# Kernel optimization log

Measured on AMD Instinct MI355X. Metric: run time of the kernel, lower is better.

Reference implementation:

```python
import jax, jax.numpy as jnp
import numpy as np

WIN = 8          # current_window
PRETRAIN = 8     # pretrain_window
HEADS = 8
SHIFT = WIN // 2 # shift_size, shift_dir = [1, 1] (shift_mode=1)
L = WIN * WIN
LOG100 = float(np.log(100.0))


def _shift_mask(H, W):
    # bands (shift_dir=[1,1], no padding). Pairs from different regions get -100.
    hr = np.repeat(np.arange(3), [H - WIN, WIN - SHIFT, SHIFT])
    wr = np.repeat(np.arange(3), [W - WIN, WIN - SHIFT, SHIFT])
    region = hr[:, None] * 3 + wr[None, :]                      # [H, W]
    reg = region.reshape(H // WIN, WIN, W // WIN, WIN)
    reg = reg.transpose(0, 2, 1, 3).reshape(-1, L)              # [nw, L]
    m = np.where(reg[:, :, None] != reg[:, None, :], -100.0, 0.0)
    return jnp.asarray(m, dtype=jnp.float32)[None, :, None]     # [1, nw, 1, L, L]


def _rel_bias(cpb_w1, cpb_b1, cpb_w2):
    # Swin-v2 continuous relative position bias (log-spaced coords + MLP).
    pos = np.stack(np.meshgrid(np.arange(WIN), np.arange(WIN), indexing='ij'), -1).reshape(L, 2)
    rc = (pos[:, None, :] - pos[None, :, :]).astype(np.float32)  # [L, L, 2]
    rc = rc / (PRETRAIN - 1) * 8.0
    rc = np.sign(rc) * np.log2(np.abs(rc) + 1.0) / np.log2(8.0)
    rc = jnp.asarray(rc)
    bias = jax.nn.relu(rc @ cpb_w1 + cpb_b1) @ cpb_w2            # [L, L, heads]
    bias = 16.0 * jax.nn.sigmoid(bias)
    return bias.transpose(2, 0, 1)                               # [heads, L, L]


def _l2n(a):
    # tf.math.l2_normalize with epsilon=1.55e-5
    return a * jax.lax.rsqrt(jnp.maximum(jnp.sum(a * a, -1, keepdims=True), 1.55e-5))


def setup_inputs() -> dict:
    key = jax.random.key(0)
    ks = jax.random.split(key, 6)
    B, H, W, C = 16, 128, 128, 256
    cpb = 512
    return {
        'x': jax.random.normal(ks[0], (B, H, W, C), jnp.float32),
        'qkv_w': jax.random.normal(ks[1], (C, 3 * C), jnp.float32) * 0.02,
        'q_bias': jnp.zeros((C,), jnp.float32),
        'v_bias': jnp.zeros((C,), jnp.float32),
        'scale': jnp.full((HEADS, 1, 1), np.log(10.0), jnp.float32),
        'cpb_w1': jax.random.normal(ks[2], (2, cpb), jnp.float32) * 0.02,
        'cpb_b1': jnp.zeros((cpb,), jnp.float32),
        'cpb_w2': jax.random.normal(ks[3], (cpb, HEADS), jnp.float32) * 0.02,
        'proj_w': jax.random.normal(ks[4], (C, C), jnp.float32) * 0.02,
        'proj_b': jnp.zeros((C,), jnp.float32),
    }


def reference(x, qkv_w, q_bias, v_bias, scale, cpb_w1, cpb_b1, cpb_w2, proj_w, proj_b):
    B, H, W, C = x.shape
    units = C // HEADS
    # qkv 1x1 conv + (q, 0, v) bias
    bias = jnp.concatenate([q_bias, jnp.zeros_like(q_bias), v_bias])
    qkv = jnp.einsum('bhwc,cd->bhwd', x, qkv_w) + bias
    # cyclic shift (H, W > window so shift is applied; no padding needed)
    qkv = jnp.roll(qkv, (-SHIFT, -SHIFT), axis=(1, 2))
    # fused window partition -> [B, nw, heads, L, 3*units]
    nh, nw = H // WIN, W // WIN
    t = qkv.reshape(B, nh, WIN, nw, WIN, HEADS, 3 * units)
    t = t.transpose(0, 1, 3, 5, 2, 4, 6).reshape(B, nh * nw, HEADS, L, 3 * units)
    q, k, v = jnp.split(t, 3, axis=-1)
    # cosine attention with clamped learned logit scale
    logit_scale = jnp.exp(jnp.minimum(scale, LOG100))            # [heads, 1, 1]
    attn = jnp.einsum('bnhld,bnhmd->bnhlm', _l2n(q) * logit_scale, _l2n(k))
    attn = attn + _rel_bias(cpb_w1, cpb_b1, cpb_w2)[None, None] + _shift_mask(H, W)
    attn = jax.nn.softmax(attn, axis=-1)
    out = jnp.einsum('bnhlm,bnhmd->bnhld', attn, v)
    # reverse partition, reverse shift, output projection
    out = out.reshape(B, nh, nw, HEADS, WIN, WIN, units)
    out = out.transpose(0, 1, 4, 2, 5, 3, 6).reshape(B, H, W, C)
    out = jnp.roll(out, (SHIFT, SHIFT), axis=(1, 2))
    return jnp.einsum('bhwc,cd->bhwd', out, proj_w) + proj_b
```

## Files before the change

### kernel.cpp

```cpp
#include <hip/hip_runtime.h>

typedef __attribute__((ext_vector_type(4))) float  f32x4;
typedef __attribute__((ext_vector_type(8))) __bf16 bf16x8;
typedef __attribute__((ext_vector_type(4))) __bf16 bf16x4;

__global__ __launch_bounds__(256) void prep_kernel(
    const float* __restrict__ qw, const float* __restrict__ pw,
    const float* __restrict__ qb, const float* __restrict__ vb,
    const float* __restrict__ w1, const float* __restrict__ b1,
    const float* __restrict__ w2,
    __bf16* __restrict__ W2, __bf16* __restrict__ Wp,
    float* __restrict__ bcat, float* __restrict__ cpbias)
{
  if (blockIdx.x < 131) {
    int i = blockIdx.x * 256 + threadIdx.x;
    if (i < 24576) {
      int h = i / 3072, rem = i - h * 3072;
      int ft = rem >> 9, rem2 = rem & 511;
      int ks = rem2 >> 6, l = rem2 & 63;
      int g = l >> 4, c = l & 15;
      int col = h * 96 + ft * 16 + c;
      bf16x8 v;
      #pragma unroll
      for (int j = 0; j < 8; ++j)
        v[j] = (__bf16)qw[(ks * 32 + g * 8 + j) * 768 + col];
      *(bf16x8*)(W2 + (size_t)i * 8) = v;
    } else if (i < 24576 + 8192) {
      int j = i - 24576;
      int wv = j >> 10, rem = j & 1023;
      int ft = rem >> 9, rem2 = rem & 511;
      int ks = rem2 >> 6, l = rem2 & 63;
      int g = l >> 4, c = l & 15;
      int col = wv * 32 + ft * 16 + c;
      bf16x8 v;
      #pragma unroll
      for (int j8 = 0; j8 < 8; ++j8)
        v[j8] = (__bf16)pw[(ks * 32 + g * 8 + j8) * 256 + col];
      *(bf16x8*)(Wp + (size_t)j * 8) = v;
    } else if (i < 24576 + 8192 + 768) {
      int cdx = i - 24576 - 8192;
      bcat[cdx] = (cdx < 256) ? qb[cdx] : ((cdx < 512) ? 0.0f : vb[cdx - 512]);
    }
  } else {
    int pair = (blockIdx.x - 131) * 256 + threadIdx.x;
    int lq = pair >> 6, mk = pair & 63;
    float d0 = (float)((lq >> 3) - (mk >> 3));
    float d1 = (float)((lq & 7) - (mk & 7));
    float v0 = d0 * (8.0f / 7.0f);
    float v1 = d1 * (8.0f / 7.0f);
    float s0 = (v0 > 0.f) ? 1.f : ((v0 < 0.f) ? -1.f : 0.f);
    float s1 = (v1 > 0.f) ? 1.f : ((v1 < 0.f) ? -1.f : 0.f);
    float r0 = s0 * log2f(fabsf(v0) + 1.0f) * (1.0f / 3.0f);
    float r1 = s1 * log2f(fabsf(v1) + 1.0f) * (1.0f / 3.0f);
    float acc[8] = {0.f, 0.f, 0.f, 0.f, 0.f, 0.f, 0.f, 0.f};
    #pragma unroll 4
    for (int j = 0; j < 512; ++j) {
      float h = fmaxf(r0 * w1[j] + r1 * w1[512 + j] + b1[j], 0.0f);
      #pragma unroll
      for (int q = 0; q < 8; ++q) acc[q] += h * w2[j * 8 + q];
    }
    #pragma unroll
    for (int q = 0; q < 8; ++q) {
      float s = 16.0f / (1.0f + __expf(-acc[q]));
      cpbias[(q * 64 + lq) * 64 + mk] = s;
    }
  }
}

__device__ __forceinline__ int win_region(int tok, int wi, int wj) {
  int r = tok >> 3, cc = tok & 7;
  int rh = (wi == 15) ? ((r < 4) ? 1 : 2) : 0;
  int rw = (wj == 15) ? ((cc < 4) ? 1 : 2) : 0;
  return rh * 3 + rw;
}

template <int FT>
__device__ __forceinline__ void qkv2(const __bf16* __restrict__ Wh,
                                     const __bf16* xs, int l, int g, int c,
                                     f32x4 (&a)[2][4])
{
  const f32x4 zz = {0.f, 0.f, 0.f, 0.f};
  #pragma unroll
  for (int ft = 0; ft < 2; ++ft)
    #pragma unroll
    for (int tt = 0; tt < 4; ++tt) a[ft][tt] = zz;
  #pragma unroll
  for (int ks = 0; ks < 8; ++ks) {
    bf16x8 w0 = *(const bf16x8*)(Wh + (size_t)(((FT + 0) * 8 + ks) * 64 + l) * 8);
    bf16x8 w1 = *(const bf16x8*)(Wh + (size_t)(((FT + 1) * 8 + ks) * 64 + l) * 8);
    #pragma unroll
    for (int tt = 0; tt < 4; ++tt) {
      int phys = (ks * 4 + g) ^ (c & 7);
      bf16x8 xf = *(const bf16x8*)&xs[(tt * 16 + c) * 256 + phys * 8];
      a[0][tt] = __builtin_amdgcn_mfma_f32_16x16x32_bf16(w0, xf, a[0][tt], 0, 0, 0);
      a[1][tt] = __builtin_amdgcn_mfma_f32_16x16x32_bf16(w1, xf, a[1][tt], 0, 0, 0);
    }
  }
}

__global__ __launch_bounds__(512, 2) void fused_kernel(
    const float* __restrict__ x, const __bf16* __restrict__ W2,
    const __bf16* __restrict__ Wp, const float* __restrict__ bcat,
    const float* __restrict__ scale, const float* __restrict__ cpb,
    const float* __restrict__ pb, float* __restrict__ outf)
{
  __shared__ __align__(16) __bf16 xs[64 * 256];
  __shared__ __align__(16) __bf16 vst[8][64 * 36];
  const f32x4 zz = {0.f, 0.f, 0.f, 0.f};

  int t = threadIdx.x;
  int h = t >> 6, l = t & 63, g = l >> 4, c = l & 15;
  int win = blockIdx.x, b = blockIdx.y;
  int wi = win >> 4, wj = win & 15;
  bool edge = (wi == 15) || (wj == 15);

  {
    int r = t >> 3;
    int q8 = t & 7;
    int ht = (wi * 8 + (r >> 3) + 4) & 127;
    int wt = (wj * 8 + (r & 7) + 4) & 127;
    const float* src = x + (size_t)((b * 128 + ht) * 128 + wt) * 256 + q8 * 32;
    #pragma unroll
    for (int q = 0; q < 4; ++q) {
      f32x4 a0 = *(const f32x4*)(src + q * 8);
      f32x4 a1 = *(const f32x4*)(src + q * 8 + 4);
      bf16x8 v;
      #pragma unroll
      for (int j = 0; j < 4; ++j) { v[j] = (__bf16)a0[j]; v[4 + j] = (__bf16)a1[j]; }
      int phys = (q8 * 4 + q) ^ (r & 7);
      *(bf16x8*)&xs[r * 256 + phys * 8] = v;
    }
  }
  __syncthreads();

  int toko[4];
  #pragma unroll
  for (int i = 0; i < 4; ++i) {
    int tok = 16 * i + c;
    int ht = (wi * 8 + (tok >> 3) + 4) & 127;
    int wt = (wj * 8 + (tok & 7) + 4) & 127;
    toko[i] = ((b * 128 + ht) * 128 + wt) * 256;
  }

  const __bf16* Wh = W2 + (size_t)h * 24576;
  float ls = __expf(fminf(scale[h], 4.6051701859880914f));

  bf16x8 qB[4], kA[4];
  {
    f32x4 a[2][4];
    qkv2<0>(Wh, xs, l, g, c, a);
    f32x4 b0 = *(const f32x4*)&bcat[h * 96 + 0  + 4 * g];
    f32x4 b1 = *(const f32x4*)&bcat[h * 96 + 16 + 4 * g];
    #pragma unroll
    for (int tt = 0; tt < 4; ++tt) {
      a[0][tt] += b0; a[1][tt] += b1;
      float s = 0.f;
      #pragma unroll
      for (int i = 0; i < 4; ++i)
        s += a[0][tt][i] * a[0][tt][i] + a[1][tt][i] * a[1][tt][i];
      s += __shfl_xor(s, 16); s += __shfl_xor(s, 32);
      float r = rsqrtf(fmaxf(s, 1.55e-5f)) * ls;
      #pragma unroll
      for (int i = 0; i < 4; ++i) {
        qB[tt][i]     = (__bf16)(a[0][tt][i] * r);
        qB[tt][4 + i] = (__bf16)(a[1][tt][i] * r);
      }
    }
  }

  {
    f32x4 a[2][4];
    qkv2<2>(Wh, xs, l, g, c, a);
    f32x4 b0 = *(const f32x4*)&bcat[h * 96 + 32 + 4 * g];
    f32x4 b1 = *(const f32x4*)&bcat[h * 96 + 48 + 4 * g];
    #pragma unroll
    for (int tt = 0; tt < 4; ++tt) {
      a[0][tt] += b0; a[1][tt] += b1;
      float s = 0.f;
      #pragma unroll
      for (int i = 0; i < 4; ++i)
        s += a[0][tt][i] * a[0][tt][i] + a[1][tt][i] * a[1][tt][i];
      s += __shfl_xor(s, 16); s += __shfl_xor(s, 32);
      float r = rsqrtf(fmaxf(s, 1.55e-5f));
      #pragma unroll
      for (int i = 0; i < 4; ++i) {
        kA[tt][i]     = (__bf16)(a[0][tt][i] * r);
        kA[tt][4 + i] = (__bf16)(a[1][tt][i] * r);
      }
    }
  }

  {
    f32x4 a[2][4];
    qkv2<4>(Wh, xs, l, g, c, a);
    __syncthreads();
    f32x4 b0 = *(const f32x4*)&bcat[h * 96 + 64 + 4 * g];
    f32x4 b1 = *(const f32x4*)&bcat[h * 96 + 80 + 4 * g];
    #pragma unroll
    for (int tt = 0; tt < 4; ++tt) {
      bf16x4 v0, v1;
      #pragma unroll
      for (int i = 0; i < 4; ++i) {
        v0[i] = (__bf16)(a[0][tt][i] + b0[i]);
        v1[i] = (__bf16)(a[1][tt][i] + b1[i]);
      }
      __bf16* vrow = &vst[h][(tt * 16 + c) * 36];
      *(bf16x4*)&vrow[4 * g]      = v0;
      *(bf16x4*)&vrow[16 + 4 * g] = v1;
    }
  }

  bf16x8 va[2][2];
  #pragma unroll
  for (int mh = 0; mh < 2; ++mh)
    #pragma unroll
    for (int kp = 0; kp < 2; ++kp)
      #pragma unroll
      for (int j = 0; j < 8; ++j)
        va[mh][kp][j] =
            vst[h][(32 * kp + 16 * (j >> 2) + 4 * g + (j & 3)) * 36 + 16 * mh + c];

  #pragma unroll
  for (int nt = 0; nt < 4; ++nt) {
    f32x4 tt4[4];
    #pragma unroll
    for (int mt = 0; mt < 4; ++mt)
      tt4[mt] = __builtin_amdgcn_mfma_f32_16x16x32_bf16(kA[mt], qB[nt], zz, 0, 0, 0);
    int q = nt * 16 + c;
    float p[16];
    #pragma unroll
    for (int mt = 0; mt < 4; ++mt) {
      f32x4 bb = *(const f32x4*)&cpb[(h * 64 + q) * 64 + mt * 16 + 4 * g];
      #pragma unroll
      for (int i = 0; i < 4; ++i) p[mt * 4 + i] = tt4[mt][i] + bb[i];
    }
    if (edge) {
      int regq = win_region(q, wi, wj);
      #pragma unroll
      for (int mt = 0; mt < 4; ++mt)
        #pragma unroll
        for (int i = 0; i < 4; ++i) {
          int k = mt * 16 + 4 * g + i;
          if (win_region(k, wi, wj) != regq) p[mt * 4 + i] -= 100.0f;
        }
    }
    float mx = -1e30f;
    #pragma unroll
    for (int j = 0; j < 16; ++j) mx = fmaxf(mx, p[j]);
    mx = fmaxf(mx, __shfl_xor(mx, 16));
    mx = fmaxf(mx, __shfl_xor(mx, 32));
    float sum = 0.f;
    #pragma unroll
    for (int j = 0; j < 16; ++j) { p[j] = __expf(p[j] - mx); sum += p[j]; }
    sum += __shfl_xor(sum, 16); sum += __shfl_xor(sum, 32);
    float rinv = 1.0f / sum;
    bf16x8 pf0, pf1;
    #pragma unroll
    for (int j = 0; j < 8; ++j) { pf0[j] = (__bf16)p[j]; pf1[j] = (__bf16)p[8 + j]; }
    #pragma unroll
    for (int mh = 0; mh < 2; ++mh) {
      f32x4 oo = __builtin_amdgcn_mfma_f32_16x16x32_bf16(va[mh][0], pf0, zz, 0, 0, 0);
      oo = __builtin_amdgcn_mfma_f32_16x16x32_bf16(va[mh][1], pf1, oo, 0, 0, 0);
      int chunk = h * 4 + 2 * mh + (g >> 1);
      int tok = nt * 16 + c;
      int phys = chunk ^ (tok & 7);
      bf16x4 ov = { (__bf16)(oo[0] * rinv), (__bf16)(oo[1] * rinv),
                    (__bf16)(oo[2] * rinv), (__bf16)(oo[3] * rinv) };
      *(bf16x4*)&xs[tok * 256 + phys * 8 + 4 * (g & 1)] = ov;
    }
  }
  __syncthreads();

  f32x4 acc2[2][4];
  #pragma unroll
  for (int ft = 0; ft < 2; ++ft)
    #pragma unroll
    for (int tt = 0; tt < 4; ++tt) acc2[ft][tt] = zz;

  const __bf16* Wph = Wp + (size_t)h * 8192;
  #pragma unroll
  for (int ks = 0; ks < 8; ++ks) {
    bf16x8 w0 = *(const bf16x8*)(Wph + (size_t)((0 * 8 + ks) * 64 + l) * 8);
    bf16x8 w1 = *(const bf16x8*)(Wph + (size_t)((1 * 8 + ks) * 64 + l) * 8);
    #pragma unroll
    for (int tt = 0; tt < 4; ++tt) {
      int phys = (ks * 4 + g) ^ (c & 7);
      bf16x8 xf = *(const bf16x8*)&xs[(tt * 16 + c) * 256 + phys * 8];
      acc2[0][tt] = __builtin_amdgcn_mfma_f32_16x16x32_bf16(w0, xf, acc2[0][tt], 0, 0, 0);
      acc2[1][tt] = __builtin_amdgcn_mfma_f32_16x16x32_bf16(w1, xf, acc2[1][tt], 0, 0, 0);
    }
  }

  #pragma unroll
  for (int ft = 0; ft < 2; ++ft) {
    f32x4 bb = *(const f32x4*)&pb[h * 32 + ft * 16 + 4 * g];
    #pragma unroll
    for (int tt = 0; tt < 4; ++tt) {
      f32x4 res = acc2[ft][tt] + bb;
      *(f32x4*)&outf[toko[tt] + h * 32 + ft * 16 + 4 * g] = res;
    }
  }
}

extern "C" void kernel_launch(void* const* d_in, const int* in_sizes, int n_in,
                              void* d_out, int out_size, void* d_ws, size_t ws_size,
                              hipStream_t stream)
{
  const float* x      = (const float*)d_in[0];
  const float* qkv_w  = (const float*)d_in[1];
  const float* q_bias = (const float*)d_in[2];
  const float* v_bias = (const float*)d_in[3];
  const float* scale  = (const float*)d_in[4];
  const float* cpb_w1 = (const float*)d_in[5];
  const float* cpb_b1 = (const float*)d_in[6];
  const float* cpb_w2 = (const float*)d_in[7];
  const float* proj_w = (const float*)d_in[8];
  const float* proj_b = (const float*)d_in[9];

  char* ws = (char*)d_ws;
  __bf16* W2   = (__bf16*)(ws);
  __bf16* Wp   = (__bf16*)(ws + 393216LL);
  float*  bcat = (float*) (ws + 524288LL);
  float*  cpb  = (float*) (ws + 527360LL);

  prep_kernel<<<147, 256, 0, stream>>>(qkv_w, proj_w, q_bias, v_bias,
                                       cpb_w1, cpb_b1, cpb_w2, W2, Wp, bcat, cpb);
  fused_kernel<<<dim3(256, 16), 512, 0, stream>>>(x, W2, Wp, bcat, scale, cpb,
                                                  proj_b, (float*)d_out);
}
```

Before: 444.8 us.

## Split each head across two waves with 1024-thread blocks, sharing K via LDS

Each attention head is now handled by two wavefronts, each owning half of the window's query tokens, so a block runs 16 waves of 1024 threads with launch bounds of one block per CU. K is no longer kept whole in one wave's registers: each wave writes its half of normalized K into a new LDS buffer, and after a barrier both waves read the full K and V. The goal is fewer registers and less serial work per wave, giving more latency hiding within a block. The cost is extra LDS traffic and space for K, W weights read twice per head, and only one resident block per CU instead of two.

```diff
diff --git a/kernel.cpp b/kernel.cpp
--- a/kernel.cpp
+++ b/kernel.cpp
@@ -77,139 +77,154 @@
 template <int FT>
 __device__ __forceinline__ void qkv2(const __bf16* __restrict__ Wh,
                                      const __bf16* xs, int l, int g, int c,
-                                     f32x4 (&a)[2][4])
+                                     int hf, f32x4 (&a)[2][2])
 {
   const f32x4 zz = {0.f, 0.f, 0.f, 0.f};
   #pragma unroll
   for (int ft = 0; ft < 2; ++ft)
     #pragma unroll
-    for (int tt = 0; tt < 4; ++tt) a[ft][tt] = zz;
+    for (int ntl = 0; ntl < 2; ++ntl) a[ft][ntl] = zz;
   #pragma unroll
   for (int ks = 0; ks < 8; ++ks) {
     bf16x8 w0 = *(const bf16x8*)(Wh + (size_t)(((FT + 0) * 8 + ks) * 64 + l) * 8);
     bf16x8 w1 = *(const bf16x8*)(Wh + (size_t)(((FT + 1) * 8 + ks) * 64 + l) * 8);
     #pragma unroll
-    for (int tt = 0; tt < 4; ++tt) {
+    for (int ntl = 0; ntl < 2; ++ntl) {
+      int tt = 2 * hf + ntl;
       int phys = (ks * 4 + g) ^ (c & 7);
       bf16x8 xf = *(const bf16x8*)&xs[(tt * 16 + c) * 256 + phys * 8];
-      a[0][tt] = __builtin_amdgcn_mfma_f32_16x16x32_bf16(w0, xf, a[0][tt], 0, 0, 0);
-      a[1][tt] = __builtin_amdgcn_mfma_f32_16x16x32_bf16(w1, xf, a[1][tt], 0, 0, 0);
-    }
-  }
-}
-
-__global__ __launch_bounds__(512, 2) void fused_kernel(
+      a[0][ntl] = __builtin_amdgcn_mfma_f32_16x16x32_bf16(w0, xf, a[0][ntl], 0, 0, 0);
+      a[1][ntl] = __builtin_amdgcn_mfma_f32_16x16x32_bf16(w1, xf, a[1][ntl], 0, 0, 0);
+    }
+  }
+}
+
+__global__ __launch_bounds__(1024, 1) void fused_kernel(
     const float* __restrict__ x, const __bf16* __restrict__ W2,
     const __bf16* __restrict__ Wp, const float* __restrict__ bcat,
     const float* __restrict__ scale, const float* __restrict__ cpb,
     const float* __restrict__ pb, float* __restrict__ outf)
 {
   __shared__ __align__(16) __bf16 xs[64 * 256];
+  __shared__ __align__(16) __bf16 kst[8][64 * 36];
   __shared__ __align__(16) __bf16 vst[8][64 * 36];
   const f32x4 zz = {0.f, 0.f, 0.f, 0.f};
 
   int t = threadIdx.x;
-  int h = t >> 6, l = t & 63, g = l >> 4, c = l & 15;
+  int wv = t >> 6, h = wv >> 1, hf = wv & 1;
+  int l = t & 63, g = l >> 4, c = l & 15;
   int win = blockIdx.x, b = blockIdx.y;
   int wi = win >> 4, wj = win & 15;
   bool edge = (wi == 15) || (wj == 15);
 
   {
-    int r = t >> 3;
-    int q8 = t & 7;
+    int r = t >> 4;
+    int sub = t & 15;
     int ht = (wi * 8 + (r >> 3) + 4) & 127;
     int wt = (wj * 8 + (r & 7) + 4) & 127;
-    const float* src = x + (size_t)((b * 128 + ht) * 128 + wt) * 256 + q8 * 32;
-    #pragma unroll
-    for (int q = 0; q < 4; ++q) {
+    const float* src = x + (size_t)((b * 128 + ht) * 128 + wt) * 256 + sub * 16;
+    #pragma unroll
+    for (int q = 0; q < 2; ++q) {
       f32x4 a0 = *(const f32x4*)(src + q * 8);
       f32x4 a1 = *(const f32x4*)(src + q * 8 + 4);
       bf16x8 v;
       #pragma unroll
       for (int j = 0; j < 4; ++j) { v[j] = (__bf16)a0[j]; v[4 + j] = (__bf16)a1[j]; }
-      int phys = (q8 * 4 + q) ^ (r & 7);
+      int phys = (sub * 2 + q) ^ (r & 7);
       *(bf16x8*)&xs[r * 256 + phys * 8] = v;
     }
   }
   __syncthreads();
 
-  int toko[4];
-  #pragma unroll
-  for (int i = 0; i < 4; ++i) {
-    int tok = 16 * i + c;
+  int toko[2];
+  #pragma unroll
+  for (int ntl = 0; ntl < 2; ++ntl) {
+    int tok = (2 * hf + ntl) * 16 + c;
     int ht = (wi * 8 + (tok >> 3) + 4) & 127;
     int wt = (wj * 8 + (tok & 7) + 4) & 127;
-    toko[i] = ((b * 128 + ht) * 128 + wt) * 256;
+    toko[ntl] = ((b * 128 + ht) * 128 + wt) * 256;
   }
 
   const __bf16* Wh = W2 + (size_t)h * 24576;
   float ls = __expf(fminf(scale[h], 4.6051701859880914f));
 
-  bf16x8 qB[4], kA[4];
+  bf16x8 qB[2];
   {
-    f32x4 a[2][4];
-    qkv2<0>(Wh, xs, l, g, c, a);
+    f32x4 a[2][2];
+    qkv2<0>(Wh, xs, l, g, c, hf, a);
     f32x4 b0 = *(const f32x4*)&bcat[h * 96 + 0  + 4 * g];
     f32x4 b1 = *(const f32x4*)&bcat[h * 96 + 16 + 4 * g];
     #pragma unroll
-    for (int tt = 0; tt < 4; ++tt) {
-      a[0][tt] += b0; a[1][tt] += b1;
+    for (int ntl = 0; ntl < 2; ++ntl) {
+      a[0][ntl] += b0; a[1][ntl] += b1;
       float s = 0.f;
       #pragma unroll
       for (int i = 0; i < 4; ++i)
-        s += a[0][tt][i] * a[0][tt][i] + a[1][tt][i] * a[1][tt][i];
+        s += a[0][ntl][i] * a[0][ntl][i] + a[1][ntl][i] * a[1][ntl][i];
       s += __shfl_xor(s, 16); s += __shfl_xor(s, 32);
       float r = rsqrtf(fmaxf(s, 1.55e-5f)) * ls;
       #pragma unroll
       for (int i = 0; i < 4; ++i) {
-        qB[tt][i]     = (__bf16)(a[0][tt][i] * r);
-        qB[tt][4 + i] = (__bf16)(a[1][tt][i] * r);
+        qB[ntl][i]     = (__bf16)(a[0][ntl][i] * r);
+        qB[ntl][4 + i] = (__bf16)(a[1][ntl][i] * r);
       }
     }
   }
 
   {
-    f32x4 a[2][4];
-    qkv2<2>(Wh, xs, l, g, c, a);
+    f32x4 a[2][2];
+    qkv2<2>(Wh, xs, l, g, c, hf, a);
     f32x4 b0 = *(const f32x4*)&bcat[h * 96 + 32 + 4 * g];
     f32x4 b1 = *(const f32x4*)&bcat[h * 96 + 48 + 4 * g];
     #pragma unroll
-    for (int tt = 0; tt < 4; ++tt) {
-      a[0][tt] += b0; a[1][tt] += b1;
+    for (int ntl = 0; ntl < 2; ++ntl) {
+      a[0][ntl] += b0; a[1][ntl] += b1;
       float s = 0.f;
       #pragma unroll
       for (int i = 0; i < 4; ++i)
-        s += a[0][tt][i] * a[0][tt][i] + a[1][tt][i] * a[1][tt][i];
+        s += a[0][ntl][i] * a[0][ntl][i] + a[1][ntl][i] * a[1][ntl][i];
       s += __shfl_xor(s, 16); s += __shfl_xor(s, 32);
       float r = rsqrtf(fmaxf(s, 1.55e-5f));
+      bf16x4 k0, k1;
       #pragma unroll
       for (int i = 0; i < 4; ++i) {
-        kA[tt][i]     = (__bf16)(a[0][tt][i] * r);
-        kA[tt][4 + i] = (__bf16)(a[1][tt][i] * r);
+        k0[i] = (__bf16)(a[0][ntl][i] * r);
+        k1[i] = (__bf16)(a[1][ntl][i] * r);
       }
+      int tok = (2 * hf + ntl) * 16 + c;
+      *(bf16x4*)&kst[h][tok * 36 + 4 * g]      = k0;
+      *(bf16x4*)&kst[h][tok * 36 + 16 + 4 * g] = k1;
     }
   }
 
   {
-    f32x4 a[2][4];
-    qkv2<4>(Wh, xs, l, g, c, a);
-    __syncthreads();
+    f32x4 a[2][2];
+    qkv2<4>(Wh, xs, l, g, c, hf, a);
     f32x4 b0 = *(const f32x4*)&bcat[h * 96 + 64 + 4 * g];
     f32x4 b1 = *(const f32x4*)&bcat[h * 96 + 80 + 4 * g];
     #pragma unroll
-    for (int tt = 0; tt < 4; ++tt) {
+    for (int ntl = 0; ntl < 2; ++ntl) {
       bf16x4 v0, v1;
       #pragma unroll
       for (int i = 0; i < 4; ++i) {
-        v0[i] = (__bf16)(a[0][tt][i] + b0[i]);
-        v1[i] = (__bf16)(a[1][tt][i] + b1[i]);
+        v0[i] = (__bf16)(a[0][ntl][i] + b0[i]);
+        v1[i] = (__bf16)(a[1][ntl][i] + b1[i]);
       }
-      __bf16* vrow = &vst[h][(tt * 16 + c) * 36];
-      *(bf16x4*)&vrow[4 * g]      = v0;
-      *(bf16x4*)&vrow[16 + 4 * g] = v1;
-    }
-  }
-
+      int tok = (2 * hf + ntl) * 16 + c;
+      *(bf16x4*)&vst[h][tok * 36 + 4 * g]      = v0;
+      *(bf16x4*)&vst[h][tok * 36 + 16 + 4 * g] = v1;
+    }
+  }
+  __syncthreads();
+
+  bf16x8 kA[4];
+  #pragma unroll
+  for (int mt = 0; mt < 4; ++mt) {
+    bf16x4 lo = *(const bf16x4*)&kst[h][(mt * 16 + c) * 36 + 4 * g];
+    bf16x4 hi = *(const bf16x4*)&kst[h][(mt * 16 + c) * 36 + 16 + 4 * g];
+    #pragma unroll
+    for (int i = 0; i < 4; ++i) { kA[mt][i] = lo[i]; kA[mt][4 + i] = hi[i]; }
+  }
   bf16x8 va[2][2];
   #pragma unroll
   for (int mh = 0; mh < 2; ++mh)
@@ -221,12 +236,12 @@
             vst[h][(32 * kp + 16 * (j >> 2) + 4 * g + (j & 3)) * 36 + 16 * mh + c];
 
   #pragma unroll
-  for (int nt = 0; nt < 4; ++nt) {
+  for (int ntl = 0; ntl < 2; ++ntl) {
     f32x4 tt4[4];
     #pragma unroll
     for (int mt = 0; mt < 4; ++mt)
-      tt4[mt] = __builtin_amdgcn_mfma_f32_16x16x32_bf16(kA[mt], qB[nt], zz, 0, 0, 0);
-    int q = nt * 16 + c;
+      tt4[mt] = __builtin_amdgcn_mfma_f32_16x16x32_bf16(kA[mt], qB[ntl], zz, 0, 0, 0);
+    int q = (2 * hf + ntl) * 16 + c;
     float p[16];
     #pragma unroll
     for (int mt = 0; mt < 4; ++mt) {
@@ -257,12 +272,12 @@
     bf16x8 pf0, pf1;
     #pragma unroll
     for (int j = 0; j < 8; ++j) { pf0[j] = (__bf16)p[j]; pf1[j] = (__bf16)p[8 + j]; }
+    int tok = q;
     #pragma unroll
     for (int mh = 0; mh < 2; ++mh) {
       f32x4 oo = __builtin_amdgcn_mfma_f32_16x16x32_bf16(va[mh][0], pf0, zz, 0, 0, 0);
       oo = __builtin_amdgcn_mfma_f32_16x16x32_bf16(va[mh][1], pf1, oo, 0, 0, 0);
       int chunk = h * 4 + 2 * mh + (g >> 1);
-      int tok = nt * 16 + c;
       int phys = chunk ^ (tok & 7);
       bf16x4 ov = { (__bf16)(oo[0] * rinv), (__bf16)(oo[1] * rinv),
                     (__bf16)(oo[2] * rinv), (__bf16)(oo[3] * rinv) };
@@ -271,11 +286,11 @@
   }
   __syncthreads();
 
-  f32x4 acc2[2][4];
+  f32x4 acc2[2][2];
   #pragma unroll
   for (int ft = 0; ft < 2; ++ft)
     #pragma unroll
-    for (int tt = 0; tt < 4; ++tt) acc2[ft][tt] = zz;
+    for (int ntl = 0; ntl < 2; ++ntl) acc2[ft][ntl] = zz;
 
   const __bf16* Wph = Wp + (size_t)h * 8192;
   #pragma unroll
@@ -283,11 +298,12 @@
     bf16x8 w0 = *(const bf16x8*)(Wph + (size_t)((0 * 8 + ks) * 64 + l) * 8);
     bf16x8 w1 = *(const bf16x8*)(Wph + (size_t)((1 * 8 + ks) * 64 + l) * 8);
     #pragma unroll
-    for (int tt = 0; tt < 4; ++tt) {
+    for (int ntl = 0; ntl < 2; ++ntl) {
+      int tok = (2 * hf + ntl) * 16 + c;
       int phys = (ks * 4 + g) ^ (c & 7);
-      bf16x8 xf = *(const bf16x8*)&xs[(tt * 16 + c) * 256 + phys * 8];
-      acc2[0][tt] = __builtin_amdgcn_mfma_f32_16x16x32_bf16(w0, xf, acc2[0][tt], 0, 0, 0);
-      acc2[1][tt] = __builtin_amdgcn_mfma_f32_16x16x32_bf16(w1, xf, acc2[1][tt], 0, 0, 0);
+      bf16x8 xf = *(const bf16x8*)&xs[tok * 256 + phys * 8];
+      acc2[0][ntl] = __builtin_amdgcn_mfma_f32_16x16x32_bf16(w0, xf, acc2[0][ntl], 0, 0, 0);
+      acc2[1][ntl] = __builtin_amdgcn_mfma_f32_16x16x32_bf16(w1, xf, acc2[1][ntl], 0, 0, 0);
     }
   }
 
@@ -295,9 +311,9 @@
   for (int ft = 0; ft < 2; ++ft) {
     f32x4 bb = *(const f32x4*)&pb[h * 32 + ft * 16 + 4 * g];
     #pragma unroll
-    for (int tt = 0; tt < 4; ++tt) {
-      f32x4 res = acc2[ft][tt] + bb;
-      *(f32x4*)&outf[toko[tt] + h * 32 + ft * 16 + 4 * g] = res;
+    for (int ntl = 0; ntl < 2; ++ntl) {
+      f32x4 res = acc2[ft][ntl] + bb;
+      *(f32x4*)&outf[toko[ntl] + h * 32 + ft * 16 + 4 * g] = res;
     }
   }
 }
@@ -325,6 +341,6 @@
 
   prep_kernel<<<147, 256, 0, stream>>>(qkv_w, proj_w, q_bias, v_bias,
                                        cpb_w1, cpb_b1, cpb_w2, W2, Wp, bcat, cpb);
-  fused_kernel<<<dim3(256, 16), 512, 0, stream>>>(x, W2, Wp, bcat, scale, cpb,
-                                                  proj_b, (float*)d_out);
-}
+  fused_kernel<<<dim3(256, 16), 1024, 0, stream>>>(x, W2, Wp, bcat, scale, cpb,
+                                                   proj_b, (float*)d_out);
+}
```

Result: faster. 419.8 us (-5.6%).
